# Kernel tuning notes

Hardware: AMD Instinct MI355X
Metric: run time of the kernel (lower is better)

## Reference

```python
import jax, jax.numpy as jnp
import numpy as np

N = 100000   # nodes
E = 1600000  # edges (avg degree 16), self-loops added in reference
H = 64       # hidden


def setup_inputs() -> dict:
    key = jax.random.key(0)
    k1, k2, k3, k4, k5 = jax.random.split(key, 5)
    x = jax.random.normal(k1, (N, H), dtype=jnp.float32)
    src = jax.random.randint(k2, (E,), 0, N, dtype=jnp.int32)
    off = jax.random.randint(k3, (E,), 1, N, dtype=jnp.int32)
    dst = (src + off) % N  # guaranteed no self-loops -> matches add_remaining_self_loops
    edge_index = jnp.stack([src, dst])  # row0 = j (source), row1 = i (target)
    # a_i, a_j: Linear(hidden, 1, bias=False) -> weight vectors of shape [H]
    w_i = jax.random.normal(k4, (H,), dtype=jnp.float32) / np.sqrt(H)
    w_j = jax.random.normal(k5, (H,), dtype=jnp.float32) / np.sqrt(H)
    return {"x": x, "edge_index": edge_index, "w_i": w_i, "w_j": w_j}


def reference(x, edge_index, w_i, w_j):
    n = x.shape[0]
    # add_remaining_self_loops: append (v, v) for every node (inputs have none)
    loops = jnp.arange(n, dtype=edge_index.dtype)
    src = jnp.concatenate([edge_index[0], loops])  # j
    dst = jnp.concatenate([edge_index[1], loops])  # i
    # per-node attention scalars, then per-edge gather
    s_i = x @ w_i  # [N]
    s_j = x @ w_j  # [N]
    e = jax.nn.leaky_relu(s_i[dst] + s_j[src], 0.01)  # [E+N]
    # segment softmax over destination node i (every segment non-empty via self-loop)
    e_max = jax.ops.segment_max(e, dst, num_segments=n)
    e_exp = jnp.exp(e - e_max[dst])
    denom = jax.ops.segment_sum(e_exp, dst, num_segments=n)
    alpha = e_exp / denom[dst]  # [E+N]
    # spmm: out[i] = sum_j alpha_ij * x[j], then ReLU
    out = jax.ops.segment_sum(alpha[:, None] * x[src], dst, num_segments=n)
    return jax.nn.relu(out)
```

## Files before the change

kernel.cpp:

```cpp
#include <hip/hip_runtime.h>

#define H 64
#define H4 16
#define H8 8
#define NBUCK 391
#define CAP 4608
#define BIN_BLOCKS 196
#define NODE_PER_BLK 16

typedef _Float16 half8 __attribute__((ext_vector_type(8)));


__global__ __launch_bounds__(1024) void gat_nodebin_kernel(
        const float* __restrict__ x,
        const float* __restrict__ w_i, const float* __restrict__ w_j,
        float* __restrict__ s_i, float* __restrict__ s_j,
        _Float16* __restrict__ xh,
        const int4* __restrict__ src4, const int4* __restrict__ dst4,
        int* __restrict__ cursor, int* __restrict__ buckets,
        int e4, int n) {
    __shared__ int hist[NBUCK];
    __shared__ int boff[NBUCK];
    __shared__ int boff0[NBUCK];
    __shared__ int gbase[NBUCK];
    __shared__ int wtot[16];
    __shared__ int stage[8192];

    int tid = threadIdx.x;
    int lane = tid & 63, wv = tid >> 6;

    if (blockIdx.x >= BIN_BLOCKS) {
        int node = (blockIdx.x - BIN_BLOCKS) * NODE_PER_BLK + wv;
        if (node >= n) return;
        float v = x[(long long)node * H + lane];
        xh[(long long)node * H + lane] = (_Float16)v;
        float a = v * w_i[lane];
        float b = v * w_j[lane];
        #pragma unroll
        for (int off = 32; off > 0; off >>= 1) {
            a += __shfl_down(a, off, 64);
            b += __shfl_down(b, off, 64);
        }
        if (lane == 0) { s_i[node] = a; s_j[node] = b; }
        return;
    }

    if (tid < NBUCK) hist[tid] = 0;
    __syncthreads();

    int4 s[2], d[2];
    bool val[2];
    #pragma unroll
    for (int r = 0; r < 2; ++r) {
        int i4 = blockIdx.x * 2048 + r * 1024 + tid;
        val[r] = (i4 < e4);
        if (val[r]) { s[r] = src4[i4]; d[r] = dst4[i4]; }
        else        { s[r] = make_int4(0,0,0,0); d[r] = make_int4(0,0,0,0); }
    }
    #pragma unroll
    for (int r = 0; r < 2; ++r) if (val[r]) {
        atomicAdd(&hist[d[r].x >> 8], 1);
        atomicAdd(&hist[d[r].y >> 8], 1);
        atomicAdd(&hist[d[r].z >> 8], 1);
        atomicAdd(&hist[d[r].w >> 8], 1);
    }
    __syncthreads();

    if (tid < NBUCK) gbase[tid] = atomicAdd(&cursor[tid], hist[tid]);

    int v = (tid < NBUCK) ? hist[tid] : 0;
    int incl = v;
    #pragma unroll
    for (int off = 1; off < 64; off <<= 1) {
        int t = __shfl_up(incl, off, 64);
        if (lane >= off) incl += t;
    }
    if (lane == 63) wtot[wv] = incl;
    __syncthreads();
    if (tid < NBUCK) {
        int wpref = 0;
        #pragma unroll
        for (int j = 0; j < 16; ++j) wpref += (j < wv) ? wtot[j] : 0;
        int excl = wpref + incl - v;
        boff[tid]  = excl;
        boff0[tid] = excl;
    }
    __syncthreads();

    #pragma unroll
    for (int r = 0; r < 2; ++r) if (val[r]) {
        int ss[4] = {s[r].x, s[r].y, s[r].z, s[r].w};
        int dd[4] = {d[r].x, d[r].y, d[r].z, d[r].w};
        #pragma unroll
        for (int c = 0; c < 4; ++c) {
            int b = dd[c] >> 8;
            int pos = atomicAdd(&boff[b], 1);
            stage[pos] = ((dd[c] & 255) << 17) | ss[c];
        }
    }
    __syncthreads();

    for (int b = wv; b < NBUCK; b += 16) {
        int sbase = boff0[b];
        int L = boff[b] - sbase;
        int gb = gbase[b];
        int* dstp = buckets + (long long)b * CAP + gb;
        for (int i = lane; i < L; i += 64)
            dstp[i] = stage[sbase + i];
    }
}

__global__ __launch_bounds__(1024) void gat_sort_kernel(
        const int* __restrict__ cursor, int* __restrict__ buckets,
        int* __restrict__ row_start, int* __restrict__ count, int n) {
    __shared__ int hist[256];
    __shared__ int offs[256];
    __shared__ int stage[CAP];
    __shared__ int stage2[CAP];
    __shared__ int wtot[4];

    int b = blockIdx.x;
    int tid = threadIdx.x;
    int cnt = cursor[b];
    int* bk = buckets + (long long)b * CAP;

    if (tid < 256) hist[tid] = 0;
    __syncthreads();

    for (int i = tid; i < cnt; i += 1024) {
        int w = bk[i];
        stage[i] = w;
        atomicAdd(&hist[(w >> 17) & 255], 1);
    }
    __syncthreads();

    int lane = tid & 63, wv = tid >> 6;
    if (tid < 256) {
        int v = hist[tid];
        int incl = v;
        #pragma unroll
        for (int off = 1; off < 64; off <<= 1) {
            int t = __shfl_up(incl, off, 64);
            if (lane >= off) incl += t;
        }
        if (lane == 63) wtot[wv] = incl;
        __syncthreads();
        int wpref = 0;
        #pragma unroll
        for (int j = 0; j < 4; ++j) wpref += (j < wv) ? wtot[j] : 0;
        int excl = wpref + incl - v;
        offs[tid] = excl;
        int node = (b << 8) + tid;
        if (node < n) {
            row_start[node] = b * CAP + excl;
            count[node] = v;
        }
    } else {
        __syncthreads();
    }
    __syncthreads();

    for (int i = tid; i < cnt; i += 1024) {
        int w = stage[i];
        int pos = atomicAdd(&offs[(w >> 17) & 255], 1);
        stage2[pos] = w & 0x1FFFF;
    }
    __syncthreads();

    for (int i = tid; i < cnt; i += 1024)
        bk[i] = stage2[i];
}

__global__ void gat_aggregate_kernel(const float4* __restrict__ x4,
                                     const half8* __restrict__ xh8,
                                     const float* __restrict__ s_i,
                                     const float* __restrict__ s_j,
                                     const int* __restrict__ row_start,
                                     const int* __restrict__ count,
                                     const int* __restrict__ csr_src,
                                     float4* __restrict__ out4, int n) {
    int node = (blockIdx.x * blockDim.x + threadIdx.x) >> 6;
    int lane = threadIdx.x & 63;
    if (node >= n) return;
    int g = lane >> 3;
    int q = lane & 7;

    float sii = s_i[node];
    int start = row_start[node];
    int cnt = count[node];

    float acc[8];
    #pragma unroll
    for (int i = 0; i < 8; ++i) acc[i] = 0.f;
    float den = 0.f;

    for (int base = 0; base < cnt; base += 64) {
        int rem = cnt - base;
        int prsrc = node;
        float wl = 0.f;
        if (lane < rem) {
            prsrc = csr_src[start + base + lane];
            float e = sii + s_j[prsrc];
            e = (e >= 0.f) ? e : 0.01f * e;
            wl = __expf(e);
        }
        int m = (rem < 64) ? rem : 64;
        int mp = (m + 15) & ~15;
        for (int k = g; k < mp; k += 16) {
            int kb = k + 8;
            int s0 = __shfl(prsrc, k, 64);
            int s1 = __shfl(prsrc, kb, 64);
            float w0 = __shfl(wl, k, 64);
            float w1 = __shfl(wl, kb, 64);
            half8 h0 = xh8[(long long)s0 * H8 + q];
            half8 h1 = xh8[(long long)s1 * H8 + q];
            #pragma unroll
            for (int i = 0; i < 8; ++i)
                acc[i] = fmaf(w0, (float)h0[i], acc[i]);
            #pragma unroll
            for (int i = 0; i < 8; ++i)
                acc[i] = fmaf(w1, (float)h1[i], acc[i]);
            den += w0 + w1;
        }
    }

    #pragma unroll
    for (int off = 8; off <= 32; off <<= 1) {
        #pragma unroll
        for (int i = 0; i < 8; ++i) acc[i] += __shfl_xor(acc[i], off, 64);
        den += __shfl_xor(den, off, 64);
    }

    if (lane < 8) {
        float sjn = s_j[node];
        float e0 = sii + sjn; e0 = (e0 >= 0.f) ? e0 : 0.01f * e0;
        float w0 = __expf(e0);
        float4 xa = x4[(long long)node * H4 + 2 * q];
        float4 xb = x4[(long long)node * H4 + 2 * q + 1];
        float dinv = 1.f / (den + w0);
        float4 oa, ob;
        oa.x = (acc[0] + w0 * xa.x) * dinv;
        oa.y = (acc[1] + w0 * xa.y) * dinv;
        oa.z = (acc[2] + w0 * xa.z) * dinv;
        oa.w = (acc[3] + w0 * xa.w) * dinv;
        ob.x = (acc[4] + w0 * xb.x) * dinv;
        ob.y = (acc[5] + w0 * xb.y) * dinv;
        ob.z = (acc[6] + w0 * xb.z) * dinv;
        ob.w = (acc[7] + w0 * xb.w) * dinv;
        oa.x = (oa.x > 0.f) ? oa.x : 0.f;
        oa.y = (oa.y > 0.f) ? oa.y : 0.f;
        oa.z = (oa.z > 0.f) ? oa.z : 0.f;
        oa.w = (oa.w > 0.f) ? oa.w : 0.f;
        ob.x = (ob.x > 0.f) ? ob.x : 0.f;
        ob.y = (ob.y > 0.f) ? ob.y : 0.f;
        ob.z = (ob.z > 0.f) ? ob.z : 0.f;
        ob.w = (ob.w > 0.f) ? ob.w : 0.f;
        out4[(long long)node * H4 + 2 * q]     = oa;
        out4[(long long)node * H4 + 2 * q + 1] = ob;
    }
}

extern "C" void kernel_launch(void* const* d_in, const int* in_sizes, int n_in,
                              void* d_out, int out_size, void* d_ws, size_t ws_size,
                              hipStream_t stream) {
    const float* x    = (const float*)d_in[0];
    const int*   edge = (const int*)  d_in[1];
    const float* w_i  = (const float*)d_in[2];
    const float* w_j  = (const float*)d_in[3];

    int n     = in_sizes[0] / H;
    int e_cnt = in_sizes[1] / 2;
    const int* src = edge;
    const int* dst = edge + e_cnt;

    float* out = (float*)d_out;

    char* ws = (char*)d_ws;
    float*    s_i       = (float*)ws;     ws += (size_t)n * 4;
    float*    s_j       = (float*)ws;     ws += (size_t)n * 4;
    int*      cursor    = (int*)ws;       ws += 512 * 4;
    int*      row_start = (int*)ws;       ws += (size_t)n * 4;
    int*      count     = (int*)ws;       ws += (size_t)n * 4;
    int*      buckets   = (int*)ws;       ws += (size_t)NBUCK * CAP * 4;
    _Float16* xh        = (_Float16*)ws;

    int e4 = e_cnt / 4;
    int node_blocks = (n + NODE_PER_BLK - 1) / NODE_PER_BLK;
    int fused_blocks = BIN_BLOCKS + node_blocks;

    hipMemsetAsync(cursor, 0, 512 * 4, stream);

    gat_nodebin_kernel<<<fused_blocks, 1024, 0, stream>>>(
        x, w_i, w_j, s_i, s_j, xh,
        (const int4*)src, (const int4*)dst, cursor, buckets, e4, n);

    gat_sort_kernel<<<NBUCK, 1024, 0, stream>>>(
        cursor, buckets, row_start, count, n);

    long long agg_threads = (long long)n * 64;
    gat_aggregate_kernel<<<(unsigned)((agg_threads + 255) / 256), 256, 0, stream>>>(
        (const float4*)x, (const half8*)xh, s_i, s_j, row_start, count, buckets,
        (float4*)out, n);
}
```

Measured before the change: 161.6 us.

## Fuse per-bucket sort into aggregation kernel using LDS-resident CSR

```diff
diff --git a/kernel.cpp b/kernel.cpp
--- a/kernel.cpp
+++ b/kernel.cpp
@@ -110,153 +110,145 @@
     }
 }
 
-__global__ __launch_bounds__(1024) void gat_sort_kernel(
-        const int* __restrict__ cursor, int* __restrict__ buckets,
-        int* __restrict__ row_start, int* __restrict__ count, int n) {
-    __shared__ int hist[256];
+__global__ __launch_bounds__(1024) void gat_agg_kernel(
+        const float4* __restrict__ x4, const half8* __restrict__ xh8,
+        const float* __restrict__ s_i, const float* __restrict__ s_j,
+        const int* __restrict__ cursor, const int* __restrict__ buckets,
+        float4* __restrict__ out4, int n) {
+    __shared__ int cnts[256];
+    __shared__ int pstart[256];
     __shared__ int offs[256];
+    __shared__ int wtot[4];
+    __shared__ float sil[256];
     __shared__ int stage[CAP];
-    __shared__ int stage2[CAP];
-    __shared__ int wtot[4];
-
+    __shared__ int srcs[CAP];
+
+    int tid = threadIdx.x;
     int b = blockIdx.x;
-    int tid = threadIdx.x;
+    int node0 = b << 8;
     int cnt = cursor[b];
-    int* bk = buckets + (long long)b * CAP;
-
-    if (tid < 256) hist[tid] = 0;
+    const int* bk = buckets + (long long)b * CAP;
+    int lane = tid & 63, wv = tid >> 6;
+
+    if (tid < 256) {
+        cnts[tid] = 0;
+        int gn = node0 + tid;
+        sil[tid] = (gn < n) ? s_i[gn] : 0.f;
+    }
     __syncthreads();
 
     for (int i = tid; i < cnt; i += 1024) {
         int w = bk[i];
         stage[i] = w;
-        atomicAdd(&hist[(w >> 17) & 255], 1);
-    }
-    __syncthreads();
-
-    int lane = tid & 63, wv = tid >> 6;
+        atomicAdd(&cnts[(w >> 17) & 255], 1);
+    }
+    __syncthreads();
+
+    int v = (tid < 256) ? cnts[tid] : 0;
+    int incl = v;
+    #pragma unroll
+    for (int off = 1; off < 64; off <<= 1) {
+        int t = __shfl_up(incl, off, 64);
+        if (lane >= off) incl += t;
+    }
+    if (tid < 256 && lane == 63) wtot[wv] = incl;
+    __syncthreads();
     if (tid < 256) {
-        int v = hist[tid];
-        int incl = v;
-        #pragma unroll
-        for (int off = 1; off < 64; off <<= 1) {
-            int t = __shfl_up(incl, off, 64);
-            if (lane >= off) incl += t;
-        }
-        if (lane == 63) wtot[wv] = incl;
-        __syncthreads();
         int wpref = 0;
         #pragma unroll
         for (int j = 0; j < 4; ++j) wpref += (j < wv) ? wtot[j] : 0;
         int excl = wpref + incl - v;
+        pstart[tid] = excl;
         offs[tid] = excl;
-        int node = (b << 8) + tid;
-        if (node < n) {
-            row_start[node] = b * CAP + excl;
-            count[node] = v;
-        }
-    } else {
-        __syncthreads();
     }
     __syncthreads();
 
     for (int i = tid; i < cnt; i += 1024) {
         int w = stage[i];
         int pos = atomicAdd(&offs[(w >> 17) & 255], 1);
-        stage2[pos] = w & 0x1FFFF;
-    }
-    __syncthreads();
-
-    for (int i = tid; i < cnt; i += 1024)
-        bk[i] = stage2[i];
-}
-
-__global__ void gat_aggregate_kernel(const float4* __restrict__ x4,
-                                     const half8* __restrict__ xh8,
-                                     const float* __restrict__ s_i,
-                                     const float* __restrict__ s_j,
-                                     const int* __restrict__ row_start,
-                                     const int* __restrict__ count,
-                                     const int* __restrict__ csr_src,
-                                     float4* __restrict__ out4, int n) {
-    int node = (blockIdx.x * blockDim.x + threadIdx.x) >> 6;
-    int lane = threadIdx.x & 63;
-    if (node >= n) return;
+        srcs[pos] = w & 0x1FFFF;
+    }
+    __syncthreads();
+
     int g = lane >> 3;
     int q = lane & 7;
-
-    float sii = s_i[node];
-    int start = row_start[node];
-    int cnt = count[node];
-
-    float acc[8];
-    #pragma unroll
-    for (int i = 0; i < 8; ++i) acc[i] = 0.f;
-    float den = 0.f;
-
-    for (int base = 0; base < cnt; base += 64) {
-        int rem = cnt - base;
-        int prsrc = node;
-        float wl = 0.f;
-        if (lane < rem) {
-            prsrc = csr_src[start + base + lane];
-            float e = sii + s_j[prsrc];
-            e = (e >= 0.f) ? e : 0.01f * e;
-            wl = __expf(e);
-        }
-        int m = (rem < 64) ? rem : 64;
-        int mp = (m + 15) & ~15;
-        for (int k = g; k < mp; k += 16) {
-            int kb = k + 8;
-            int s0 = __shfl(prsrc, k, 64);
-            int s1 = __shfl(prsrc, kb, 64);
-            float w0 = __shfl(wl, k, 64);
-            float w1 = __shfl(wl, kb, 64);
-            half8 h0 = xh8[(long long)s0 * H8 + q];
-            half8 h1 = xh8[(long long)s1 * H8 + q];
+    for (int j = 0; j < 16; ++j) {
+        int nd = (wv << 4) + j;
+        int gn = node0 + nd;
+        if (gn >= n) break;
+        int start = pstart[nd];
+        int ecnt = cnts[nd];
+        float sii = sil[nd];
+
+        float acc[8];
+        #pragma unroll
+        for (int i = 0; i < 8; ++i) acc[i] = 0.f;
+        float den = 0.f;
+
+        for (int base = 0; base < ecnt; base += 64) {
+            int rem = ecnt - base;
+            int prsrc = gn;
+            float wl = 0.f;
+            if (lane < rem) {
+                prsrc = srcs[start + base + lane];
+                float e = sii + s_j[prsrc];
+                e = (e >= 0.f) ? e : 0.01f * e;
+                wl = __expf(e);
+            }
+            int m = (rem < 64) ? rem : 64;
+            int mp = (m + 15) & ~15;
+            for (int k = g; k < mp; k += 16) {
+                int kb = k + 8;
+                int s0 = __shfl(prsrc, k, 64);
+                int s1 = __shfl(prsrc, kb, 64);
+                float w0 = __shfl(wl, k, 64);
+                float w1 = __shfl(wl, kb, 64);
+                half8 h0 = xh8[(long long)s0 * H8 + q];
+                half8 h1 = xh8[(long long)s1 * H8 + q];
+                #pragma unroll
+                for (int i = 0; i < 8; ++i)
+                    acc[i] = fmaf(w0, (float)h0[i], acc[i]);
+                #pragma unroll
+                for (int i = 0; i < 8; ++i)
+                    acc[i] = fmaf(w1, (float)h1[i], acc[i]);
+                den += w0 + w1;
+            }
+        }
+
+        #pragma unroll
+        for (int off = 8; off <= 32; off <<= 1) {
             #pragma unroll
-            for (int i = 0; i < 8; ++i)
-                acc[i] = fmaf(w0, (float)h0[i], acc[i]);
-            #pragma unroll
-            for (int i = 0; i < 8; ++i)
-                acc[i] = fmaf(w1, (float)h1[i], acc[i]);
-            den += w0 + w1;
-        }
-    }
-
-    #pragma unroll
-    for (int off = 8; off <= 32; off <<= 1) {
-        #pragma unroll
-        for (int i = 0; i < 8; ++i) acc[i] += __shfl_xor(acc[i], off, 64);
-        den += __shfl_xor(den, off, 64);
-    }
-
-    if (lane < 8) {
-        float sjn = s_j[node];
-        float e0 = sii + sjn; e0 = (e0 >= 0.f) ? e0 : 0.01f * e0;
-        float w0 = __expf(e0);
-        float4 xa = x4[(long long)node * H4 + 2 * q];
-        float4 xb = x4[(long long)node * H4 + 2 * q + 1];
-        float dinv = 1.f / (den + w0);
-        float4 oa, ob;
-        oa.x = (acc[0] + w0 * xa.x) * dinv;
-        oa.y = (acc[1] + w0 * xa.y) * dinv;
-        oa.z = (acc[2] + w0 * xa.z) * dinv;
-        oa.w = (acc[3] + w0 * xa.w) * dinv;
-        ob.x = (acc[4] + w0 * xb.x) * dinv;
-        ob.y = (acc[5] + w0 * xb.y) * dinv;
-        ob.z = (acc[6] + w0 * xb.z) * dinv;
-        ob.w = (acc[7] + w0 * xb.w) * dinv;
-        oa.x = (oa.x > 0.f) ? oa.x : 0.f;
-        oa.y = (oa.y > 0.f) ? oa.y : 0.f;
-        oa.z = (oa.z > 0.f) ? oa.z : 0.f;
-        oa.w = (oa.w > 0.f) ? oa.w : 0.f;
-        ob.x = (ob.x > 0.f) ? ob.x : 0.f;
-        ob.y = (ob.y > 0.f) ? ob.y : 0.f;
-        ob.z = (ob.z > 0.f) ? ob.z : 0.f;
-        ob.w = (ob.w > 0.f) ? ob.w : 0.f;
-        out4[(long long)node * H4 + 2 * q]     = oa;
-        out4[(long long)node * H4 + 2 * q + 1] = ob;
+            for (int i = 0; i < 8; ++i) acc[i] += __shfl_xor(acc[i], off, 64);
+            den += __shfl_xor(den, off, 64);
+        }
+
+        if (lane < 8) {
+            float sjn = s_j[gn];
+            float e0 = sii + sjn; e0 = (e0 >= 0.f) ? e0 : 0.01f * e0;
+            float w0 = __expf(e0);
+            float4 xa = x4[(long long)gn * H4 + 2 * q];
+            float4 xb = x4[(long long)gn * H4 + 2 * q + 1];
+            float dinv = 1.f / (den + w0);
+            float4 oa, ob;
+            oa.x = (acc[0] + w0 * xa.x) * dinv;
+            oa.y = (acc[1] + w0 * xa.y) * dinv;
+            oa.z = (acc[2] + w0 * xa.z) * dinv;
+            oa.w = (acc[3] + w0 * xa.w) * dinv;
+            ob.x = (acc[4] + w0 * xb.x) * dinv;
+            ob.y = (acc[5] + w0 * xb.y) * dinv;
+            ob.z = (acc[6] + w0 * xb.z) * dinv;
+            ob.w = (acc[7] + w0 * xb.w) * dinv;
+            oa.x = (oa.x > 0.f) ? oa.x : 0.f;
+            oa.y = (oa.y > 0.f) ? oa.y : 0.f;
+            oa.z = (oa.z > 0.f) ? oa.z : 0.f;
+            oa.w = (oa.w > 0.f) ? oa.w : 0.f;
+            ob.x = (ob.x > 0.f) ? ob.x : 0.f;
+            ob.y = (ob.y > 0.f) ? ob.y : 0.f;
+            ob.z = (ob.z > 0.f) ? ob.z : 0.f;
+            ob.w = (ob.w > 0.f) ? ob.w : 0.f;
+            out4[(long long)gn * H4 + 2 * q]     = oa;
+            out4[(long long)gn * H4 + 2 * q + 1] = ob;
+        }
     }
 }
 
@@ -276,13 +268,11 @@
     float* out = (float*)d_out;
 
     char* ws = (char*)d_ws;
-    float*    s_i       = (float*)ws;     ws += (size_t)n * 4;
-    float*    s_j       = (float*)ws;     ws += (size_t)n * 4;
-    int*      cursor    = (int*)ws;       ws += 512 * 4;
-    int*      row_start = (int*)ws;       ws += (size_t)n * 4;
-    int*      count     = (int*)ws;       ws += (size_t)n * 4;
-    int*      buckets   = (int*)ws;       ws += (size_t)NBUCK * CAP * 4;
-    _Float16* xh        = (_Float16*)ws;
+    float*    s_i     = (float*)ws;     ws += (size_t)n * 4;
+    float*    s_j     = (float*)ws;     ws += (size_t)n * 4;
+    int*      cursor  = (int*)ws;       ws += 512 * 4;
+    int*      buckets = (int*)ws;       ws += (size_t)NBUCK * CAP * 4;
+    _Float16* xh      = (_Float16*)ws;
 
     int e4 = e_cnt / 4;
     int node_blocks = (n + NODE_PER_BLK - 1) / NODE_PER_BLK;
@@ -294,11 +284,7 @@
         x, w_i, w_j, s_i, s_j, xh,
         (const int4*)src, (const int4*)dst, cursor, buckets, e4, n);
 
-    gat_sort_kernel<<<NBUCK, 1024, 0, stream>>>(
-        cursor, buckets, row_start, count, n);
-
-    long long agg_threads = (long long)n * 64;
-    gat_aggregate_kernel<<<(unsigned)((agg_threads + 255) / 256), 256, 0, stream>>>(
-        (const float4*)x, (const half8*)xh, s_i, s_j, row_start, count, buckets,
+    gat_agg_kernel<<<NBUCK, 1024, 0, stream>>>(
+        (const float4*)x, (const half8*)xh, s_i, s_j, cursor, buckets,
         (float4*)out, n);
 }
```

Result: slower. 168.6 us (+4.3%).

## Shrink binning blocks to 512 threads and flatten the bucket flush loop

Applied to the files above, without the earlier changes.

```diff
diff --git a/kernel.cpp b/kernel.cpp
--- a/kernel.cpp
+++ b/kernel.cpp
@@ -5,13 +5,13 @@
 #define H8 8
 #define NBUCK 391
 #define CAP 4608
-#define BIN_BLOCKS 196
-#define NODE_PER_BLK 16
+#define BIN_BLOCKS 782
+#define NODE_PER_BLK 8
 
 typedef _Float16 half8 __attribute__((ext_vector_type(8)));
 
 
-__global__ __launch_bounds__(1024) void gat_nodebin_kernel(
+__global__ __launch_bounds__(512) void gat_nodebin_kernel(
         const float* __restrict__ x,
         const float* __restrict__ w_i, const float* __restrict__ w_j,
         float* __restrict__ s_i, float* __restrict__ s_j,
@@ -23,8 +23,9 @@
     __shared__ int boff[NBUCK];
     __shared__ int boff0[NBUCK];
     __shared__ int gbase[NBUCK];
-    __shared__ int wtot[16];
-    __shared__ int stage[8192];
+    __shared__ int wtot[8];
+    __shared__ int stage[2048];
+    __shared__ unsigned short sbuck[2048];
 
     int tid = threadIdx.x;
     int lane = tid & 63, wv = tid >> 6;
@@ -48,21 +49,15 @@
     if (tid < NBUCK) hist[tid] = 0;
     __syncthreads();
 
-    int4 s[2], d[2];
-    bool val[2];
-    #pragma unroll
-    for (int r = 0; r < 2; ++r) {
-        int i4 = blockIdx.x * 2048 + r * 1024 + tid;
-        val[r] = (i4 < e4);
-        if (val[r]) { s[r] = src4[i4]; d[r] = dst4[i4]; }
-        else        { s[r] = make_int4(0,0,0,0); d[r] = make_int4(0,0,0,0); }
-    }
-    #pragma unroll
-    for (int r = 0; r < 2; ++r) if (val[r]) {
-        atomicAdd(&hist[d[r].x >> 8], 1);
-        atomicAdd(&hist[d[r].y >> 8], 1);
-        atomicAdd(&hist[d[r].z >> 8], 1);
-        atomicAdd(&hist[d[r].w >> 8], 1);
+    int i4 = blockIdx.x * 512 + tid;
+    bool val = (i4 < e4);
+    int4 s = val ? src4[i4] : make_int4(0, 0, 0, 0);
+    int4 d = val ? dst4[i4] : make_int4(0, 0, 0, 0);
+    if (val) {
+        atomicAdd(&hist[d.x >> 8], 1);
+        atomicAdd(&hist[d.y >> 8], 1);
+        atomicAdd(&hist[d.z >> 8], 1);
+        atomicAdd(&hist[d.w >> 8], 1);
     }
     __syncthreads();
 
@@ -80,33 +75,30 @@
     if (tid < NBUCK) {
         int wpref = 0;
         #pragma unroll
-        for (int j = 0; j < 16; ++j) wpref += (j < wv) ? wtot[j] : 0;
+        for (int j = 0; j < 8; ++j) wpref += (j < wv) ? wtot[j] : 0;
         int excl = wpref + incl - v;
         boff[tid]  = excl;
         boff0[tid] = excl;
     }
     __syncthreads();
 
-    #pragma unroll
-    for (int r = 0; r < 2; ++r) if (val[r]) {
-        int ss[4] = {s[r].x, s[r].y, s[r].z, s[r].w};
-        int dd[4] = {d[r].x, d[r].y, d[r].z, d[r].w};
+    if (val) {
+        int ss[4] = {s.x, s.y, s.z, s.w};
+        int dd[4] = {d.x, d.y, d.z, d.w};
         #pragma unroll
         for (int c = 0; c < 4; ++c) {
             int b = dd[c] >> 8;
             int pos = atomicAdd(&boff[b], 1);
             stage[pos] = ((dd[c] & 255) << 17) | ss[c];
-        }
-    }
-    __syncthreads();
-
-    for (int b = wv; b < NBUCK; b += 16) {
-        int sbase = boff0[b];
-        int L = boff[b] - sbase;
-        int gb = gbase[b];
-        int* dstp = buckets + (long long)b * CAP + gb;
-        for (int i = lane; i < L; i += 64)
-            dstp[i] = stage[sbase + i];
+            sbuck[pos] = (unsigned short)b;
+        }
+    }
+    __syncthreads();
+
+    int tot = boff[NBUCK - 1];
+    for (int idx = tid; idx < tot; idx += 512) {
+        int b = sbuck[idx];
+        buckets[(long long)b * CAP + gbase[b] + (idx - boff0[b])] = stage[idx];
     }
 }
 
@@ -135,16 +127,16 @@
     __syncthreads();
 
     int lane = tid & 63, wv = tid >> 6;
+    int v = (tid < 256) ? hist[tid] : 0;
+    int incl = v;
+    #pragma unroll
+    for (int off = 1; off < 64; off <<= 1) {
+        int t = __shfl_up(incl, off, 64);
+        if (lane >= off) incl += t;
+    }
+    if (tid < 256 && lane == 63) wtot[wv] = incl;
+    __syncthreads();
     if (tid < 256) {
-        int v = hist[tid];
-        int incl = v;
-        #pragma unroll
-        for (int off = 1; off < 64; off <<= 1) {
-            int t = __shfl_up(incl, off, 64);
-            if (lane >= off) incl += t;
-        }
-        if (lane == 63) wtot[wv] = incl;
-        __syncthreads();
         int wpref = 0;
         #pragma unroll
         for (int j = 0; j < 4; ++j) wpref += (j < wv) ? wtot[j] : 0;
@@ -155,8 +147,6 @@
             row_start[node] = b * CAP + excl;
             count[node] = v;
         }
-    } else {
-        __syncthreads();
     }
     __syncthreads();
 
@@ -290,7 +280,7 @@
 
     hipMemsetAsync(cursor, 0, 512 * 4, stream);
 
-    gat_nodebin_kernel<<<fused_blocks, 1024, 0, stream>>>(
+    gat_nodebin_kernel<<<fused_blocks, 512, 0, stream>>>(
         x, w_i, w_j, s_i, s_j, xh,
         (const int4*)src, (const int4*)dst, cursor, buckets, e4, n);
 
```

Result: slower. 169.3 us (+4.8%).

## Pack four nodes per wavefront in aggregation and batch eight gathers per lane

Applied to the files above, without the earlier changes.

```diff
diff --git a/kernel.cpp b/kernel.cpp
--- a/kernel.cpp
+++ b/kernel.cpp
@@ -135,16 +135,16 @@
     __syncthreads();
 
     int lane = tid & 63, wv = tid >> 6;
+    int v = (tid < 256) ? hist[tid] : 0;
+    int incl = v;
+    #pragma unroll
+    for (int off = 1; off < 64; off <<= 1) {
+        int t = __shfl_up(incl, off, 64);
+        if (lane >= off) incl += t;
+    }
+    if (tid < 256 && lane == 63) wtot[wv] = incl;
+    __syncthreads();
     if (tid < 256) {
-        int v = hist[tid];
-        int incl = v;
-        #pragma unroll
-        for (int off = 1; off < 64; off <<= 1) {
-            int t = __shfl_up(incl, off, 64);
-            if (lane >= off) incl += t;
-        }
-        if (lane == 63) wtot[wv] = incl;
-        __syncthreads();
         int wpref = 0;
         #pragma unroll
         for (int j = 0; j < 4; ++j) wpref += (j < wv) ? wtot[j] : 0;
@@ -155,8 +155,6 @@
             row_start[node] = b * CAP + excl;
             count[node] = v;
         }
-    } else {
-        __syncthreads();
     }
     __syncthreads();
 
@@ -171,67 +169,68 @@
         bk[i] = stage2[i];
 }
 
-__global__ void gat_aggregate_kernel(const float4* __restrict__ x4,
-                                     const half8* __restrict__ xh8,
-                                     const float* __restrict__ s_i,
-                                     const float* __restrict__ s_j,
-                                     const int* __restrict__ row_start,
-                                     const int* __restrict__ count,
-                                     const int* __restrict__ csr_src,
-                                     float4* __restrict__ out4, int n) {
-    int node = (blockIdx.x * blockDim.x + threadIdx.x) >> 6;
+__global__ __launch_bounds__(256) void gat_aggregate_kernel(
+        const float4* __restrict__ x4,
+        const half8* __restrict__ xh8,
+        const float* __restrict__ s_i,
+        const float* __restrict__ s_j,
+        const int* __restrict__ row_start,
+        const int* __restrict__ count,
+        const int* __restrict__ csr_src,
+        float4* __restrict__ out4, int n) {
+    int wid = (blockIdx.x * blockDim.x + threadIdx.x) >> 6;
     int lane = threadIdx.x & 63;
-    if (node >= n) return;
-    int g = lane >> 3;
+    int sub = lane >> 4;
+    int l16 = lane & 15;
+    int g2 = l16 >> 3;
     int q = lane & 7;
 
-    float sii = s_i[node];
-    int start = row_start[node];
-    int cnt = count[node];
+    int node = wid * 4 + sub;
+    bool vnode = (node < n);
+    int nsafe = vnode ? node : 0;
+    float sii = s_i[nsafe];
+    int start = vnode ? row_start[nsafe] : 0;
+    int cnt = vnode ? count[nsafe] : 0;
 
     float acc[8];
     #pragma unroll
     for (int i = 0; i < 8; ++i) acc[i] = 0.f;
     float den = 0.f;
 
-    for (int base = 0; base < cnt; base += 64) {
+    for (int base = 0; base < cnt; base += 16) {
         int rem = cnt - base;
-        int prsrc = node;
+        int prsrc = nsafe;
         float wl = 0.f;
-        if (lane < rem) {
-            prsrc = csr_src[start + base + lane];
+        if (l16 < rem) {
+            prsrc = csr_src[start + base + l16];
             float e = sii + s_j[prsrc];
             e = (e >= 0.f) ? e : 0.01f * e;
             wl = __expf(e);
         }
-        int m = (rem < 64) ? rem : 64;
-        int mp = (m + 15) & ~15;
-        for (int k = g; k < mp; k += 16) {
-            int kb = k + 8;
-            int s0 = __shfl(prsrc, k, 64);
-            int s1 = __shfl(prsrc, kb, 64);
-            float w0 = __shfl(wl, k, 64);
-            float w1 = __shfl(wl, kb, 64);
-            half8 h0 = xh8[(long long)s0 * H8 + q];
-            half8 h1 = xh8[(long long)s1 * H8 + q];
+        int sb[8]; float wb[8]; half8 hv[8];
+        #pragma unroll
+        for (int j = 0; j < 8; ++j) {
+            int k = (sub << 4) + g2 + 2 * j;
+            sb[j] = __shfl(prsrc, k, 64);
+            wb[j] = __shfl(wl, k, 64);
+        }
+        #pragma unroll
+        for (int j = 0; j < 8; ++j)
+            hv[j] = xh8[(long long)sb[j] * H8 + q];
+        #pragma unroll
+        for (int j = 0; j < 8; ++j) {
             #pragma unroll
             for (int i = 0; i < 8; ++i)
-                acc[i] = fmaf(w0, (float)h0[i], acc[i]);
-            #pragma unroll
-            for (int i = 0; i < 8; ++i)
-                acc[i] = fmaf(w1, (float)h1[i], acc[i]);
-            den += w0 + w1;
-        }
-    }
-
-    #pragma unroll
-    for (int off = 8; off <= 32; off <<= 1) {
-        #pragma unroll
-        for (int i = 0; i < 8; ++i) acc[i] += __shfl_xor(acc[i], off, 64);
-        den += __shfl_xor(den, off, 64);
-    }
-
-    if (lane < 8) {
+                acc[i] = fmaf(wb[j], (float)hv[j][i], acc[i]);
+            den += wb[j];
+        }
+    }
+
+    #pragma unroll
+    for (int i = 0; i < 8; ++i) acc[i] += __shfl_xor(acc[i], 8, 64);
+    den += __shfl_xor(den, 8, 64);
+
+    if (vnode && g2 == 0) {
         float sjn = s_j[node];
         float e0 = sii + sjn; e0 = (e0 >= 0.f) ? e0 : 0.01f * e0;
         float w0 = __expf(e0);
@@ -297,7 +296,8 @@
     gat_sort_kernel<<<NBUCK, 1024, 0, stream>>>(
         cursor, buckets, row_start, count, n);
 
-    long long agg_threads = (long long)n * 64;
+    int waves = (n + 3) / 4;
+    long long agg_threads = (long long)waves * 64;
     gat_aggregate_kernel<<<(unsigned)((agg_threads + 255) / 256), 256, 0, stream>>>(
         (const float4*)x, (const half8*)xh, s_i, s_j, row_start, count, buckets,
         (float4*)out, n);
```

After: 150.5 us. 1.07x faster.
